# Optimization experiments

Measured on AMD Instinct MI355X. Metric: run time of the kernel, lower is better.

The kernel has to match this reference:

```python
import jax, jax.numpy as jnp
import numpy as np

B, H, N, F, P, NODE = 64, 168, 512, 8, 24, 0


def _lstm(x, k, rk, b, return_sequences):
    # x: (B, T, Fin); keras LSTM gate order i, f, g(c), o
    Bx = x.shape[0]
    U = rk.shape[0]
    h0 = jnp.zeros((Bx, U), x.dtype)

    def step(carry, xt):
        h, c = carry
        z = xt @ k + h @ rk + b
        i, f, g, o = jnp.split(z, 4, axis=-1)
        c = jax.nn.sigmoid(f) * c + jax.nn.sigmoid(i) * jnp.tanh(g)
        h = jax.nn.sigmoid(o) * jnp.tanh(c)
        return (h, c), h

    (_, _), hs = jax.lax.scan(step, (h0, h0), jnp.swapaxes(x, 0, 1))
    return jnp.swapaxes(hs, 0, 1) if return_sequences else hs[-1]


def _node_summaries(inputs):
    # inputs: (B, H, N, F). Per-(b,n) temporal stats over H of feature 0.
    x0 = inputs[..., 0]                      # (B, H, N)
    mean_full = x0.mean(axis=1)              # (B, N)
    mean_half = x0[:, H // 2:].mean(axis=1)
    std_full = x0.std(axis=1)                # population std (ddof=0), like tf
    std_half = x0[:, H // 2:].std(axis=1)
    c = x0 - mean_full[:, None, :]
    m2 = (c * c).mean(axis=1)
    m3 = (c ** 3).mean(axis=1)
    m4 = (c ** 4).mean(axis=1)
    skew = jnp.nan_to_num(m3 / m2 ** 1.5)    # scipy.stats.skew (biased)
    kurt = jnp.nan_to_num(m4 / (m2 * m2) - 3.0)  # scipy Fisher kurtosis
    t = jnp.arange(H, dtype=x0.dtype)
    tc = t - t.mean()
    slope = jnp.nan_to_num(jnp.einsum('h,bhn->bn', tc, x0) / (tc * tc).sum())
    return jnp.stack([mean_full, mean_half, std_full, std_half, skew, kurt, slope], axis=2)  # (B, N, 7)


def reference(inputs, adj, w_gcn1, b_gcn1, w_gcn2, b_gcn2, w_conv1, b_conv1,
              w_conv2, b_conv2, k_lstm1, rk_lstm1, b_lstm1, k_lstm2, rk_lstm2,
              b_lstm2, w_out, b_out):
    nf = _node_summaries(inputs)                                   # (B, N, 7)
    # GraphConv: relu(A @ X @ W + b)
    h = jax.nn.relu(jnp.einsum('nm,bmc->bnc', adj, nf @ w_gcn1) + b_gcn1)
    g = jax.nn.relu(jnp.einsum('nm,bmc->bnc', adj, h @ w_gcn2) + b_gcn2)   # (B, N, 16)
    # Conv1D channels_first: channels = N, steps = 16
    dn = ('NCH', 'HIO', 'NCH')
    c1 = jax.lax.conv_general_dilated(g, w_conv1, (1,), 'SAME', dimension_numbers=dn) + b_conv1[None, :, None]  # (B,4,16)
    p = c1.reshape(B, 4, 8, 2).mean(axis=-1)                        # AveragePooling1D(2)  (B,4,8)
    c2 = jax.lax.conv_general_dilated(p, w_conv2, (1,), 'SAME', dimension_numbers=dn) + b_conv2[None, :, None]  # (B,4,8)
    gcn_out = jnp.concatenate([c2.reshape(B, -1), p.reshape(B, -1)], axis=-1)  # skip connection, (B, 64)
    # LSTM stack on the selected node's time series
    seq = inputs[:, :, NODE, :]                                     # (B, H, F)
    l1 = _lstm(seq, k_lstm1, rk_lstm1, b_lstm1, True)
    l2 = _lstm(l1, k_lstm2, rk_lstm2, b_lstm2, False)               # (B, 128)
    out = jnp.concatenate([gcn_out, l2], axis=-1)                   # (B, 192); dropout is identity at inference
    return out @ w_out + b_out                                      # (B, P)


def setup_inputs() -> dict:
    key = jax.random.key(0)
    ks = jax.random.split(key, 16)
    s = 0.05
    return {
        'inputs': jax.random.normal(ks[0], (B, H, N, F), jnp.float32),
        'adj': jax.random.uniform(ks[1], (N, N), jnp.float32) / N,
        'w_gcn1': jax.random.normal(ks[2], (7, 32), jnp.float32) * s,
        'b_gcn1': jnp.zeros((32,), jnp.float32),
        'w_gcn2': jax.random.normal(ks[3], (32, 16), jnp.float32) * s,
        'b_gcn2': jnp.zeros((16,), jnp.float32),
        'w_conv1': jax.random.normal(ks[4], (3, N, 4), jnp.float32) * s,
        'b_conv1': jnp.zeros((4,), jnp.float32),
        'w_conv2': jax.random.normal(ks[5], (3, 4, 4), jnp.float32) * s,
        'b_conv2': jnp.zeros((4,), jnp.float32),
        'k_lstm1': jax.random.normal(ks[6], (F, 512), jnp.float32) * s,
        'rk_lstm1': jax.random.normal(ks[7], (128, 512), jnp.float32) * s,
        'b_lstm1': jnp.zeros((512,), jnp.float32),
        'k_lstm2': jax.random.normal(ks[8], (128, 512), jnp.float32) * s,
        'rk_lstm2': jax.random.normal(ks[9], (128, 512), jnp.float32) * s,
        'b_lstm2': jnp.zeros((512,), jnp.float32),
        'w_out': jax.random.normal(ks[10], (192, P), jnp.float32) * s,
        'b_out': jnp.zeros((P,), jnp.float32),
    }
```

## Files before the change

kernel.cpp:

```cpp
#include <hip/hip_runtime.h>
#include <cstdint>
#include <cstddef>

#define BB 64
#define HH 168
#define NN 512
#define FF 8
#define UL 128
#define GD 512

__device__ __forceinline__ float sigf(float x){ return 1.0f/(1.0f+__expf(-x)); }
__device__ __forceinline__ float tanhfast(float x){ return 1.0f - 2.0f/(1.0f+__expf(2.0f*x)); }

__global__ __launch_bounds__(256) void k_sum(const float* __restrict__ in, float* __restrict__ ps){
  int bid = blockIdx.x;
  int b = bid>>2, nh = (bid>>1)&1, hh = bid&1;
  int n = nh*256 + threadIdx.x;
  int h0 = hh*84;
  const float* p = in + ((size_t)(b*HH + h0)*NN + n)*FF;
  float s1=0.f,s2=0.f,s3=0.f,s4=0.f,st=0.f;
  #pragma unroll 4
  for(int h=0;h<84;++h){
    float x = p[(size_t)h*NN*FF];
    float hc = (float)(h+h0) - 83.5f;
    s1 += x;
    float x2 = x*x;
    s2 += x2;
    s3 += x2*x;
    s4 += x2*x2;
    st += hc*x;
  }
  float* o = ps + ((size_t)((b*NN+n)*2 + hh))*8;
  o[0]=s1; o[1]=s2; o[2]=s3; o[3]=s4; o[4]=st;
}

__global__ __launch_bounds__(256) void k_sumc(const float* __restrict__ ps, float* __restrict__ nf){
  int idx = blockIdx.x*256 + threadIdx.x;
  const float* a = ps + (size_t)idx*16;
  const float* c2 = a + 8;
  float s1 = a[0]+c2[0], s2 = a[1]+c2[1], s3 = a[2]+c2[2], s4 = a[3]+c2[3], st = a[4]+c2[4];
  float s1h = c2[0], s2h = c2[1];
  const float iH = 1.0f/168.0f, iHh = 1.0f/84.0f;
  float mean = s1*iH, meanh = s1h*iHh;
  float ex2 = s2*iH, ex3 = s3*iH, ex4 = s4*iH;
  float m2 = ex2 - mean*mean;
  float m3 = ex3 - 3.0f*mean*ex2 + 2.0f*mean*mean*mean;
  float m4 = ex4 - 4.0f*mean*ex3 + 6.0f*mean*mean*ex2 - 3.0f*mean*mean*mean*mean;
  m2 = fmaxf(m2, 0.0f);
  float stdf = sqrtf(m2);
  float m2h = fmaxf(s2h*iHh - meanh*meanh, 0.0f);
  float stdh = sqrtf(m2h);
  float denom = m2*stdf;
  float skew = denom > 0.0f ? m3/denom : 0.0f;
  float kurt = m2 > 0.0f ? (m4/(m2*m2) - 3.0f) : 0.0f;
  float slope = st * (1.0f/395122.0f);
  float* o = nf + (size_t)idx*7;
  o[0]=mean; o[1]=meanh; o[2]=stdf; o[3]=stdh; o[4]=skew; o[5]=kurt; o[6]=slope;
}

__global__ __launch_bounds__(256) void k_gcn1(const float* __restrict__ nf, const float* __restrict__ adj,
        const float* __restrict__ w1, const float* __restrict__ b1, float* __restrict__ h1){
  __shared__ float t_s[NN*32];
  __shared__ float adj_s[128*68];
  int b = blockIdx.x>>2, n0 = (blockIdx.x&3)*128;
  int tid = threadIdx.x;

  {
    int c = tid&31;
    float w1c[7];
    #pragma unroll
    for(int k=0;k<7;++k) w1c[k] = w1[k*32+c];
    for(int idx=tid; idx<NN*32; idx+=256){
      int m = idx>>5;
      const float* nfp = nf + (size_t)(b*NN+m)*7;
      float acc = 0.f;
      #pragma unroll
      for(int k=0;k<7;++k) acc += nfp[k]*w1c[k];
      t_s[idx] = acc;
    }
  }
  int c2 = tid&15, nl = tid>>4;
  float acc[8][2];
  #pragma unroll
  for(int j=0;j<8;++j){acc[j][0]=0.f;acc[j][1]=0.f;}
  for(int mt=0; mt<8; ++mt){
    __syncthreads();
    for(int idx=tid; idx<128*64; idx+=256){
      int r = idx>>6, cc = idx&63;
      adj_s[r*68+cc] = adj[(size_t)(n0+r)*NN + mt*64 + cc];
    }
    __syncthreads();
    for(int mm=0; mm<64; mm+=4){
      float2 tv[4];
      #pragma unroll
      for(int q=0;q<4;++q) tv[q] = *(const float2*)&t_s[(mt*64+mm+q)*32 + 2*c2];
      #pragma unroll
      for(int j=0;j<8;++j){
        float4 a4 = *(const float4*)&adj_s[(nl+16*j)*68 + mm];
        acc[j][0] += a4.x*tv[0].x + a4.y*tv[1].x + a4.z*tv[2].x + a4.w*tv[3].x;
        acc[j][1] += a4.x*tv[0].y + a4.y*tv[1].y + a4.z*tv[2].y + a4.w*tv[3].y;
      }
    }
  }
  float bb0 = b1[2*c2], bb1 = b1[2*c2+1];
  #pragma unroll
  for(int j=0;j<8;++j){
    int n = n0 + nl + 16*j;
    float2 v;
    v.x = fmaxf(acc[j][0]+bb0, 0.0f);
    v.y = fmaxf(acc[j][1]+bb1, 0.0f);
    *(float2*)&h1[(size_t)(b*NN+n)*32 + 2*c2] = v;
  }
}

__global__ __launch_bounds__(256) void k_gcn2(const float* __restrict__ h1, const float* __restrict__ adj,
        const float* __restrict__ w2, const float* __restrict__ b2, float* __restrict__ g){
  __shared__ float t_s[NN*16];
  __shared__ float adj_s[128*68];
  int b = blockIdx.x>>2, n0 = (blockIdx.x&3)*128;
  int tid = threadIdx.x;
  {
    int jh = tid&7;
    float w2c0[32], w2c1[32];
    #pragma unroll
    for(int c=0;c<32;++c){ w2c0[c] = w2[c*16+2*jh]; w2c1[c] = w2[c*16+2*jh+1]; }
    for(int idx=tid; idx<NN*8; idx+=256){
      int m = idx>>3;
      const float4* hp = (const float4*)(h1 + (size_t)(b*NN+m)*32);
      float a0=0.f, a1=0.f;
      #pragma unroll
      for(int q=0;q<8;++q){
        float4 hv = hp[q];
        a0 += hv.x*w2c0[4*q] + hv.y*w2c0[4*q+1] + hv.z*w2c0[4*q+2] + hv.w*w2c0[4*q+3];
        a1 += hv.x*w2c1[4*q] + hv.y*w2c1[4*q+1] + hv.z*w2c1[4*q+2] + hv.w*w2c1[4*q+3];
      }
      t_s[m*16+2*jh] = a0;
      t_s[m*16+2*jh+1] = a1;
    }
  }
  int j = tid&15, nl = tid>>4;
  float acc[8];
  #pragma unroll
  for(int q=0;q<8;++q) acc[q]=0.f;
  for(int mt=0; mt<8; ++mt){
    __syncthreads();
    for(int idx=tid; idx<128*64; idx+=256){
      int r = idx>>6, cc = idx&63;
      adj_s[r*68+cc] = adj[(size_t)(n0+r)*NN + mt*64 + cc];
    }
    __syncthreads();
    for(int mm=0; mm<64; mm+=4){
      float tv[4];
      #pragma unroll
      for(int q=0;q<4;++q) tv[q] = t_s[(mt*64+mm+q)*16 + j];
      #pragma unroll
      for(int q=0;q<8;++q){
        float4 a4 = *(const float4*)&adj_s[(nl+16*q)*68 + mm];
        acc[q] += a4.x*tv[0] + a4.y*tv[1] + a4.z*tv[2] + a4.w*tv[3];
      }
    }
  }
  float bbj = b2[j];
  #pragma unroll
  for(int q=0;q<8;++q){
    int n = n0 + nl + 16*q;
    g[(size_t)(b*NN+n)*16 + j] = fmaxf(acc[q]+bbj, 0.0f);
  }
}

__global__ __launch_bounds__(64) void k_conv(const float* __restrict__ g, const float* __restrict__ wc1,
        const float* __restrict__ bc1, const float* __restrict__ wc2, const float* __restrict__ bc2,
        float* __restrict__ feat){
  __shared__ float g_s[NN*16];
  __shared__ float c1_s[4][16];
  __shared__ float p_s[4][8];
  int b = blockIdx.x, tid = threadIdx.x;
  for(int idx=tid; idx<NN*16; idx+=64) g_s[idx] = g[(size_t)b*NN*16 + idx];
  __syncthreads();
  {
    int o = tid>>4, x = tid&15;
    float acc = bc1[o];
    for(int k=0;k<3;++k){
      int xx = x + k - 1;
      if(xx>=0 && xx<16){
        for(int c=0;c<NN;++c) acc += g_s[c*16+xx]*wc1[(size_t)(k*NN+c)*4+o];
      }
    }
    c1_s[o][x] = acc;
  }
  __syncthreads();
  if(tid<32){
    int oo = tid>>3, xp = tid&7;
    float pv = 0.5f*(c1_s[oo][2*xp]+c1_s[oo][2*xp+1]);
    p_s[oo][xp] = pv;
    feat[b*192 + 32 + oo*8 + xp] = pv;
  }
  __syncthreads();
  if(tid<32){
    int oo = tid>>3, x2 = tid&7;
    float a2 = bc2[oo];
    #pragma unroll
    for(int k=0;k<3;++k){
      int xx = x2 + k - 1;
      if(xx>=0 && xx<8){
        #pragma unroll
        for(int c=0;c<4;++c) a2 += p_s[c][xx]*wc2[(k*4+c)*4+oo];
      }
    }
    feat[b*192 + oo*8 + x2] = a2;
  }
}

__global__ __launch_bounds__(512) void k_lstm1(const float* __restrict__ in, const float* __restrict__ k1,
        const float* __restrict__ rk1, const float* __restrict__ b1, float* __restrict__ l1){
  __shared__ float seq_s[HH*FF];
  __shared__ float h_s[UL];
  __shared__ float a_s[GD];
  int b = blockIdx.x, u = threadIdx.x;
  float wk[FF], wr[UL];
  #pragma unroll
  for(int f=0;f<FF;++f) wk[f] = k1[f*GD+u];
  #pragma unroll
  for(int j=0;j<UL;++j) wr[j] = rk1[j*GD+u];
  float bz = b1[u];
  for(int idx=u; idx<HH*FF; idx+=GD)
    seq_s[idx] = in[(size_t)(b*HH + (idx>>3))*NN*FF + (idx&7)];
  if(u<UL) h_s[u]=0.0f;
  float c = 0.0f;
  __syncthreads();
  int gate = u>>7;
  for(int t=0;t<HH;++t){
    float z0 = bz, z1 = 0.f, z2 = 0.f, z3 = 0.f;
    #pragma unroll
    for(int f=0;f<FF;f+=2){ z0 += seq_s[t*FF+f]*wk[f]; z1 += seq_s[t*FF+f+1]*wk[f+1]; }
    const float4* h4 = (const float4*)h_s;
    #pragma unroll
    for(int q=0;q<UL/4;++q){
      float4 hv = h4[q];
      z0 += hv.x*wr[4*q];
      z1 += hv.y*wr[4*q+1];
      z2 += hv.z*wr[4*q+2];
      z3 += hv.w*wr[4*q+3];
    }
    float z = (z0+z1)+(z2+z3);
    a_s[u] = (gate==2) ? tanhfast(z) : sigf(z);
    __syncthreads();
    if(u<UL){
      float ia = a_s[u], fa = a_s[UL+u], ga = a_s[2*UL+u], oa = a_s[3*UL+u];
      c = fa*c + ia*ga;
      float hn = oa*tanhfast(c);
      h_s[u] = hn;
      l1[((size_t)b*HH + t)*UL + u] = hn;
    }
    __syncthreads();
  }
}

__global__ __launch_bounds__(256) void k_zin2(const float* __restrict__ l1, const float* __restrict__ k2,
        const float* __restrict__ b2, float* __restrict__ zin){
  __shared__ float l_s[21*UL];
  int b = blockIdx.x>>3, t0 = (blockIdx.x&7)*21;
  int tid = threadIdx.x;
  for(int idx=tid; idx<21*UL; idx+=256)
    l_s[idx] = l1[((size_t)b*HH + t0 + (idx>>7))*UL + (idx&127)];
  __syncthreads();
  float acc0[21], acc1[21];
  #pragma unroll
  for(int q=0;q<21;++q){acc0[q]=0.f;acc1[q]=0.f;}
  for(int j=0;j<UL;++j){
    float kv0 = k2[j*GD + tid];
    float kv1 = k2[j*GD + tid + 256];
    #pragma unroll
    for(int q=0;q<21;++q){
      float lv = l_s[q*UL + j];
      acc0[q] += lv*kv0;
      acc1[q] += lv*kv1;
    }
  }
  float bb0 = b2[tid], bb1 = b2[tid+256];
  #pragma unroll
  for(int q=0;q<21;++q){
    zin[((size_t)b*HH + t0 + q)*GD + tid]       = acc0[q] + bb0;
    zin[((size_t)b*HH + t0 + q)*GD + tid + 256] = acc1[q] + bb1;
  }
}

__global__ __launch_bounds__(512) void k_lstm2(const float* __restrict__ zin, const float* __restrict__ rk2,
        float* __restrict__ feat){
  __shared__ float h_s[UL];
  __shared__ float a_s[GD];
  int b = blockIdx.x, u = threadIdx.x;
  float wr[UL];
  #pragma unroll
  for(int j=0;j<UL;++j) wr[j] = rk2[j*GD+u];
  if(u<UL) h_s[u]=0.0f;
  float c = 0.0f;
  __syncthreads();
  int gate = u>>7;
  for(int t=0;t<HH;++t){
    float z0 = zin[((size_t)b*HH+t)*GD + u], z1 = 0.f, z2 = 0.f, z3 = 0.f;
    const float4* h4 = (const float4*)h_s;
    #pragma unroll
    for(int q=0;q<UL/4;++q){
      float4 hv = h4[q];
      z0 += hv.x*wr[4*q];
      z1 += hv.y*wr[4*q+1];
      z2 += hv.z*wr[4*q+2];
      z3 += hv.w*wr[4*q+3];
    }
    float z = (z0+z1)+(z2+z3);
    a_s[u] = (gate==2) ? tanhfast(z) : sigf(z);
    __syncthreads();
    if(u<UL){
      float ia = a_s[u], fa = a_s[UL+u], ga = a_s[2*UL+u], oa = a_s[3*UL+u];
      c = fa*c + ia*ga;
      float hn = oa*tanhfast(c);
      h_s[u] = hn;
      if(t==HH-1) feat[b*192 + 64 + u] = hn;
    }
    __syncthreads();
  }
}

__global__ __launch_bounds__(256) void k_out(const float* __restrict__ feat, const float* __restrict__ wo,
        const float* __restrict__ bo, float* __restrict__ out){
  int idx = blockIdx.x*256 + threadIdx.x;
  if(idx >= BB*24) return;
  int b = idx/24, p = idx - b*24;
  float a0 = bo[p], a1 = 0.f, a2 = 0.f, a3 = 0.f;
  const float* f = feat + b*192;
  for(int k=0;k<192;k+=4){
    a0 += f[k]*wo[k*24+p];
    a1 += f[k+1]*wo[(k+1)*24+p];
    a2 += f[k+2]*wo[(k+2)*24+p];
    a3 += f[k+3]*wo[(k+3)*24+p];
  }
  out[idx] = (a0+a1)+(a2+a3);
}

extern "C" void kernel_launch(void* const* d_in, const int* in_sizes, int n_in,
                              void* d_out, int out_size, void* d_ws, size_t ws_size,
                              hipStream_t stream){
  const float* inp = (const float*)d_in[0];
  const float* adj = (const float*)d_in[1];
  const float* w1  = (const float*)d_in[2];
  const float* b1  = (const float*)d_in[3];
  const float* w2  = (const float*)d_in[4];
  const float* b2  = (const float*)d_in[5];
  const float* wc1 = (const float*)d_in[6];
  const float* bc1 = (const float*)d_in[7];
  const float* wc2 = (const float*)d_in[8];
  const float* bc2 = (const float*)d_in[9];
  const float* k1  = (const float*)d_in[10];
  const float* rk1 = (const float*)d_in[11];
  const float* bl1 = (const float*)d_in[12];
  const float* k2  = (const float*)d_in[13];
  const float* rk2 = (const float*)d_in[14];
  const float* bl2 = (const float*)d_in[15];
  const float* wo  = (const float*)d_in[16];
  const float* bo  = (const float*)d_in[17];
  float* out = (float*)d_out;
  float* ws = (float*)d_ws;

  float* ps   = ws;
  float* nf   = ps + 524288;
  float* h1   = nf + 229376;
  float* g    = h1 + 1048576;
  float* feat = g  + 524288;
  float* l1   = feat + 12288;
  float* zin  = l1 + 1376256;

  k_sum  <<<dim3(256), dim3(256), 0, stream>>>(inp, ps);
  k_sumc <<<dim3(128), dim3(256), 0, stream>>>(ps, nf);
  k_gcn1 <<<dim3(256), dim3(256), 0, stream>>>(nf, adj, w1, b1, h1);
  k_gcn2 <<<dim3(256), dim3(256), 0, stream>>>(h1, adj, w2, b2, g);
  k_conv <<<dim3(64),  dim3(64),  0, stream>>>(g, wc1, bc1, wc2, bc2, feat);
  k_lstm1<<<dim3(64),  dim3(512), 0, stream>>>(inp, k1, rk1, bl1, l1);
  k_zin2 <<<dim3(512), dim3(256), 0, stream>>>(l1, k2, bl2, zin);
  k_lstm2<<<dim3(64),  dim3(512), 0, stream>>>(zin, rk2, feat);
  k_out  <<<dim3(6),   dim3(256), 0, stream>>>(feat, wo, bo, out);
}
```

Before: 513.9 us.

## Broadcast LSTM hidden state via readlane with SGPR FMAs and split conv reduction

```diff
diff --git a/kernel.cpp b/kernel.cpp
--- a/kernel.cpp
+++ b/kernel.cpp
@@ -11,6 +11,10 @@
 
 __device__ __forceinline__ float sigf(float x){ return 1.0f/(1.0f+__expf(-x)); }
 __device__ __forceinline__ float tanhfast(float x){ return 1.0f - 2.0f/(1.0f+__expf(2.0f*x)); }
+__device__ __forceinline__ float rdlane(float v, int l){
+  return __uint_as_float(__builtin_amdgcn_readlane(__float_as_uint(v), l));
+}
+#define SFMAC(acc, s, w) asm("v_fmac_f32 %0, %1, %2" : "+v"(acc) : "s"(s), "v"(w))
 
 __global__ __launch_bounds__(256) void k_sum(const float* __restrict__ in, float* __restrict__ ps){
   int bid = blockIdx.x;
@@ -64,7 +68,6 @@
   __shared__ float adj_s[128*68];
   int b = blockIdx.x>>2, n0 = (blockIdx.x&3)*128;
   int tid = threadIdx.x;
-
   {
     int c = tid&31;
     float w1c[7];
@@ -168,25 +171,36 @@
   }
 }
 
-__global__ __launch_bounds__(64) void k_conv(const float* __restrict__ g, const float* __restrict__ wc1,
+__global__ __launch_bounds__(256) void k_conv(const float* __restrict__ g, const float* __restrict__ wc1,
         const float* __restrict__ bc1, const float* __restrict__ wc2, const float* __restrict__ bc2,
         float* __restrict__ feat){
   __shared__ float g_s[NN*16];
+  __shared__ float w1_s[3*NN*4];
+  __shared__ float c1p[4][4][16];
   __shared__ float c1_s[4][16];
   __shared__ float p_s[4][8];
   int b = blockIdx.x, tid = threadIdx.x;
-  for(int idx=tid; idx<NN*16; idx+=64) g_s[idx] = g[(size_t)b*NN*16 + idx];
+  for(int idx=tid; idx<NN*16; idx+=256) g_s[idx] = g[(size_t)b*NN*16 + idx];
+  for(int idx=tid; idx<3*NN*4; idx+=256) w1_s[idx] = wc1[idx];
   __syncthreads();
   {
-    int o = tid>>4, x = tid&15;
-    float acc = bc1[o];
+    int q = tid>>6, p = tid&63, o = p>>4, x = p&15;
+    int c0 = q*128;
+    float acc = 0.f;
+    #pragma unroll
     for(int k=0;k<3;++k){
       int xx = x + k - 1;
       if(xx>=0 && xx<16){
-        for(int c=0;c<NN;++c) acc += g_s[c*16+xx]*wc1[(size_t)(k*NN+c)*4+o];
+        #pragma unroll 4
+        for(int c=c0;c<c0+128;++c) acc += g_s[c*16+xx]*w1_s[(k*NN+c)*4+o];
       }
     }
-    c1_s[o][x] = acc;
+    c1p[q][o][x] = acc;
+  }
+  __syncthreads();
+  if(tid<64){
+    int o = tid>>4, x = tid&15;
+    c1_s[o][x] = c1p[0][o][x]+c1p[1][o][x]+c1p[2][o][x]+c1p[3][o][x] + bc1[o];
   }
   __syncthreads();
   if(tid<32){
@@ -211,46 +225,56 @@
   }
 }
 
-__global__ __launch_bounds__(512) void k_lstm1(const float* __restrict__ in, const float* __restrict__ k1,
+__global__ __launch_bounds__(256,1) void k_lstm1(const float* __restrict__ in, const float* __restrict__ k1,
         const float* __restrict__ rk1, const float* __restrict__ b1, float* __restrict__ l1){
   __shared__ float seq_s[HH*FF];
   __shared__ float h_s[UL];
   __shared__ float a_s[GD];
-  int b = blockIdx.x, u = threadIdx.x;
-  float wk[FF], wr[UL];
-  #pragma unroll
-  for(int f=0;f<FF;++f) wk[f] = k1[f*GD+u];
-  #pragma unroll
-  for(int j=0;j<UL;++j) wr[j] = rk1[j*GD+u];
-  float bz = b1[u];
-  for(int idx=u; idx<HH*FF; idx+=GD)
+  int b = blockIdx.x, tid = threadIdx.x;
+  int lane = tid & 63;
+  float wrA[UL], wrB[UL], wkA[FF], wkB[FF];
+  #pragma unroll
+  for(int j=0;j<UL;++j){ wrA[j] = rk1[j*GD+tid]; wrB[j] = rk1[j*GD+tid+256]; }
+  #pragma unroll
+  for(int f=0;f<FF;++f){ wkA[f] = k1[f*GD+tid]; wkB[f] = k1[f*GD+tid+256]; }
+  float bzA = b1[tid], bzB = b1[tid+256];
+  for(int idx=tid; idx<HH*FF; idx+=256)
     seq_s[idx] = in[(size_t)(b*HH + (idx>>3))*NN*FF + (idx&7)];
-  if(u<UL) h_s[u]=0.0f;
+  if(tid<UL) h_s[tid]=0.0f;
   float c = 0.0f;
   __syncthreads();
-  int gate = u>>7;
+  #pragma unroll 1
   for(int t=0;t<HH;++t){
-    float z0 = bz, z1 = 0.f, z2 = 0.f, z3 = 0.f;
-    #pragma unroll
-    for(int f=0;f<FF;f+=2){ z0 += seq_s[t*FF+f]*wk[f]; z1 += seq_s[t*FF+f+1]*wk[f+1]; }
-    const float4* h4 = (const float4*)h_s;
-    #pragma unroll
-    for(int q=0;q<UL/4;++q){
-      float4 hv = h4[q];
-      z0 += hv.x*wr[4*q];
-      z1 += hv.y*wr[4*q+1];
-      z2 += hv.z*wr[4*q+2];
-      z3 += hv.w*wr[4*q+3];
-    }
-    float z = (z0+z1)+(z2+z3);
-    a_s[u] = (gate==2) ? tanhfast(z) : sigf(z);
-    __syncthreads();
-    if(u<UL){
-      float ia = a_s[u], fa = a_s[UL+u], ga = a_s[2*UL+u], oa = a_s[3*UL+u];
+    float4 x0 = *(const float4*)&seq_s[t*FF];
+    float4 x1 = *(const float4*)&seq_s[t*FF+4];
+    float zA = bzA + x0.x*wkA[0]+x0.y*wkA[1]+x0.z*wkA[2]+x0.w*wkA[3]
+                   + x1.x*wkA[4]+x1.y*wkA[5]+x1.z*wkA[6]+x1.w*wkA[7];
+    float zB = bzB + x0.x*wkB[0]+x0.y*wkB[1]+x0.z*wkB[2]+x0.w*wkB[3]
+                   + x1.x*wkB[4]+x1.y*wkB[5]+x1.z*wkB[6]+x1.w*wkB[7];
+    float2 hv = *(const float2*)&h_s[2*lane];
+    float a0=0.f,a1=0.f,bb0=0.f,bb1=0.f;
+    #pragma unroll
+    for(int l=0;l<64;++l){
+      float se = rdlane(hv.x, l);
+      float so = rdlane(hv.y, l);
+      SFMAC(a0, se, wrA[2*l]);
+      SFMAC(a1, so, wrA[2*l+1]);
+      SFMAC(bb0, se, wrB[2*l]);
+      SFMAC(bb1, so, wrB[2*l+1]);
+    }
+    float zz0 = zA + (a0+a1);
+    float zz1 = zB + (bb0+bb1);
+    float actA = sigf(zz0);
+    float actB = (tid<UL) ? tanhfast(zz1) : sigf(zz1);
+    a_s[tid] = actA;
+    a_s[256+tid] = actB;
+    __syncthreads();
+    if(tid<UL){
+      float ia=a_s[tid], fa=a_s[UL+tid], ga=a_s[2*UL+tid], oa=a_s[3*UL+tid];
       c = fa*c + ia*ga;
       float hn = oa*tanhfast(c);
-      h_s[u] = hn;
-      l1[((size_t)b*HH + t)*UL + u] = hn;
+      h_s[tid] = hn;
+      l1[((size_t)b*HH + t)*UL + tid] = hn;
     }
     __syncthreads();
   }
@@ -267,14 +291,14 @@
   float acc0[21], acc1[21];
   #pragma unroll
   for(int q=0;q<21;++q){acc0[q]=0.f;acc1[q]=0.f;}
-  for(int j=0;j<UL;++j){
-    float kv0 = k2[j*GD + tid];
-    float kv1 = k2[j*GD + tid + 256];
+  for(int j=0;j<UL;j+=4){
+    float kv00=k2[j*GD+tid],     kv01=k2[(j+1)*GD+tid],     kv02=k2[(j+2)*GD+tid],     kv03=k2[(j+3)*GD+tid];
+    float kv10=k2[j*GD+tid+256], kv11=k2[(j+1)*GD+tid+256], kv12=k2[(j+2)*GD+tid+256], kv13=k2[(j+3)*GD+tid+256];
     #pragma unroll
     for(int q=0;q<21;++q){
-      float lv = l_s[q*UL + j];
-      acc0[q] += lv*kv0;
-      acc1[q] += lv*kv1;
+      float4 lv = *(const float4*)&l_s[q*UL + j];
+      acc0[q] += lv.x*kv00 + lv.y*kv01 + lv.z*kv02 + lv.w*kv03;
+      acc1[q] += lv.x*kv10 + lv.y*kv11 + lv.z*kv12 + lv.w*kv13;
     }
   }
   float bb0 = b2[tid], bb1 = b2[tid+256];
@@ -285,40 +309,54 @@
   }
 }
 
-__global__ __launch_bounds__(512) void k_lstm2(const float* __restrict__ zin, const float* __restrict__ rk2,
+__global__ __launch_bounds__(256,1) void k_lstm2(const float* __restrict__ zin, const float* __restrict__ rk2,
         float* __restrict__ feat){
   __shared__ float h_s[UL];
   __shared__ float a_s[GD];
-  int b = blockIdx.x, u = threadIdx.x;
-  float wr[UL];
-  #pragma unroll
-  for(int j=0;j<UL;++j) wr[j] = rk2[j*GD+u];
-  if(u<UL) h_s[u]=0.0f;
+  int b = blockIdx.x, tid = threadIdx.x;
+  int lane = tid & 63;
+  float wrA[UL], wrB[UL];
+  #pragma unroll
+  for(int j=0;j<UL;++j){ wrA[j] = rk2[j*GD+tid]; wrB[j] = rk2[j*GD+tid+256]; }
+  if(tid<UL) h_s[tid]=0.0f;
   float c = 0.0f;
-  __syncthreads();
-  int gate = u>>7;
+  float zA = zin[((size_t)b*HH)*GD + tid];
+  float zB = zin[((size_t)b*HH)*GD + tid + 256];
+  __syncthreads();
+  #pragma unroll 1
   for(int t=0;t<HH;++t){
-    float z0 = zin[((size_t)b*HH+t)*GD + u], z1 = 0.f, z2 = 0.f, z3 = 0.f;
-    const float4* h4 = (const float4*)h_s;
-    #pragma unroll
-    for(int q=0;q<UL/4;++q){
-      float4 hv = h4[q];
-      z0 += hv.x*wr[4*q];
-      z1 += hv.y*wr[4*q+1];
-      z2 += hv.z*wr[4*q+2];
-      z3 += hv.w*wr[4*q+3];
-    }
-    float z = (z0+z1)+(z2+z3);
-    a_s[u] = (gate==2) ? tanhfast(z) : sigf(z);
-    __syncthreads();
-    if(u<UL){
-      float ia = a_s[u], fa = a_s[UL+u], ga = a_s[2*UL+u], oa = a_s[3*UL+u];
+    float nzA = 0.f, nzB = 0.f;
+    if(t+1<HH){
+      nzA = zin[((size_t)b*HH+t+1)*GD + tid];
+      nzB = zin[((size_t)b*HH+t+1)*GD + tid + 256];
+    }
+    float2 hv = *(const float2*)&h_s[2*lane];
+    float a0=0.f,a1=0.f,bb0=0.f,bb1=0.f;
+    #pragma unroll
+    for(int l=0;l<64;++l){
+      float se = rdlane(hv.x, l);
+      float so = rdlane(hv.y, l);
+      SFMAC(a0, se, wrA[2*l]);
+      SFMAC(a1, so, wrA[2*l+1]);
+      SFMAC(bb0, se, wrB[2*l]);
+      SFMAC(bb1, so, wrB[2*l+1]);
+    }
+    float zz0 = zA + (a0+a1);
+    float zz1 = zB + (bb0+bb1);
+    float actA = sigf(zz0);
+    float actB = (tid<UL) ? tanhfast(zz1) : sigf(zz1);
+    a_s[tid] = actA;
+    a_s[256+tid] = actB;
+    __syncthreads();
+    if(tid<UL){
+      float ia=a_s[tid], fa=a_s[UL+tid], ga=a_s[2*UL+tid], oa=a_s[3*UL+tid];
       c = fa*c + ia*ga;
       float hn = oa*tanhfast(c);
-      h_s[u] = hn;
-      if(t==HH-1) feat[b*192 + 64 + u] = hn;
-    }
-    __syncthreads();
+      h_s[tid] = hn;
+      if(t==HH-1) feat[b*192 + 64 + tid] = hn;
+    }
+    __syncthreads();
+    zA = nzA; zB = nzB;
   }
 }
 
@@ -374,9 +412,9 @@
   k_sumc <<<dim3(128), dim3(256), 0, stream>>>(ps, nf);
   k_gcn1 <<<dim3(256), dim3(256), 0, stream>>>(nf, adj, w1, b1, h1);
   k_gcn2 <<<dim3(256), dim3(256), 0, stream>>>(h1, adj, w2, b2, g);
-  k_conv <<<dim3(64),  dim3(64),  0, stream>>>(g, wc1, bc1, wc2, bc2, feat);
-  k_lstm1<<<dim3(64),  dim3(512), 0, stream>>>(inp, k1, rk1, bl1, l1);
+  k_conv <<<dim3(64),  dim3(256), 0, stream>>>(g, wc1, bc1, wc2, bc2, feat);
+  k_lstm1<<<dim3(64),  dim3(256), 0, stream>>>(inp, k1, rk1, bl1, l1);
   k_zin2 <<<dim3(512), dim3(256), 0, stream>>>(l1, k2, bl2, zin);
-  k_lstm2<<<dim3(64),  dim3(512), 0, stream>>>(zin, rk2, feat);
+  k_lstm2<<<dim3(64),  dim3(256), 0, stream>>>(zin, rk2, feat);
   k_out  <<<dim3(6),   dim3(256), 0, stream>>>(feat, wo, bo, out);
 }
```

After: 695.7 us. 1.35x slower.
